# Optimization experiments

Measured on AMD Instinct MI355X. Metric: run time of the kernel, lower is better.

## Reference

```python
import jax, jax.numpy as jnp
import numpy as np

TOL = 5            # proximity_tolerance
DECAY = 0.8        # distance_decay
SWITCH_W = 20.0    # switch_loss_weight


def setup_inputs() -> dict:
    key = jax.random.key(0)
    k1, k2 = jax.random.split(key)
    B, S, C = 512, 8192, 4
    logits = jax.random.normal(k1, (B, S, C), dtype=jnp.float32)
    labels = jax.random.randint(k2, (B, S), 0, 4, dtype=jnp.int32)
    class_weights = jnp.array([1.0, 1.0, SWITCH_W, SWITCH_W], dtype=jnp.float32)
    return {"logits": logits, "labels": labels, "class_weights": class_weights}


def _nearest_dist(mask):
    """Per row: distance from each position to the nearest True in `mask`.
    Returns a large value (> S) where the row has no True. mask: [B, S] bool."""
    B, S = mask.shape
    idx = jnp.arange(S, dtype=jnp.int32)
    big = jnp.int32(4 * S)
    # index of nearest True at-or-before each position (forward cummax)
    prev = jax.lax.cummax(jnp.where(mask, idx, -big), axis=1)
    # index of nearest True at-or-after each position (backward cummin)
    nxt = jnp.flip(jax.lax.cummin(jnp.flip(jnp.where(mask, idx, 3 * big), axis=1), axis=1), axis=1)
    return jnp.minimum(idx - prev, nxt - idx)  # [B, S] int32


def reference(logits, labels, class_weights):
    B, S, C = logits.shape
    safe = jnp.where(labels < 0, 0, labels)  # handle ignore_index=-100
    logp = jax.nn.log_softmax(logits, axis=-1)
    nll = -jnp.take_along_axis(logp, safe[..., None], axis=-1)[..., 0]
    # torch F.cross_entropy(weight=w, reduction='none'): weight[y] * nll, 0 at ignore_index
    ce = jnp.where(labels < 0, 0.0, nll * class_weights[safe])  # [B, S]

    preds = jnp.argmax(logits, axis=-1)

    for c in (2, 3):  # switch-to-auto, switch-to-allo
        tmask = labels == c
        pmask = preds == c
        # predicted switches near (0 < d <= tol) a true switch of same type -> decay
        d_pt = _nearest_dist(tmask)  # dist to nearest true switch (big if none)
        near = (d_pt > 0) & (d_pt <= TOL)
        decay = jnp.where(pmask & near,
                          DECAY ** jnp.minimum(d_pt, TOL).astype(jnp.float32),
                          1.0)
        # true switches: x2 if no predicted switch of this type in the row,
        # x1.5 if nearest predicted switch is farther than tol
        d_tp = _nearest_dist(pmask)  # dist to nearest predicted switch
        any_pred = jnp.any(pmask, axis=1, keepdims=True)
        tfac = jnp.where(tmask,
                         jnp.where(any_pred,
                                   jnp.where(d_tp > TOL, 1.5, 1.0),
                                   2.0),
                         1.0)
        ce = ce * decay * tfac

    valid = (labels >= 0).astype(jnp.float32)
    return (ce * valid).sum() / jnp.maximum(valid.sum(), 1.0)
```

## Files before the change

kernel.cpp:

```cpp
#include <hip/hip_runtime.h>


#define S_LEN 8192
#define NTHREADS 1024
#define NITER (S_LEN / NTHREADS)
#define NWORDS (S_LEN / 32)
#define NWAVES (NTHREADS / 64)

__device__ inline unsigned win11(const unsigned* m, int pos) {
    int bse = pos - 5;
    int j = bse >> 5;
    int off = bse & 31;
    unsigned lo = (j >= 0) ? m[j] : 0u;
    unsigned hi = (j < NWORDS - 1) ? m[j + 1] : 0u;
    unsigned long long c = (unsigned long long)lo | ((unsigned long long)hi << 32);
    return (unsigned)((c >> off) & 0x7FFull);
}

__device__ inline float prox_factor(unsigned tw, unsigned pw, bool anyp) {
    bool tm = (tw >> 5) & 1u;
    bool pm = (pw >> 5) & 1u;
    float f = 1.0f;
    unsigned tn = tw & ~(1u << 5);
    if (pm && !tm && tn) {
        if      (tn & 0x050u) f = 0.8f;
        else if (tn & 0x088u) f = 0.64f;
        else if (tn & 0x104u) f = 0.512f;
        else if (tn & 0x202u) f = 0.4096f;
        else                  f = 0.32768f;
    }
    if (tm) {
        f *= anyp ? (pw ? 1.0f : 1.5f) : 2.0f;
    }
    return f;
}

__global__ __launch_bounds__(NTHREADS)
void prox_loss_main(const float* __restrict__ logits,
                    const int* __restrict__ labels,
                    const float* __restrict__ cw,
                    float* __restrict__ acc) {
    __shared__ float ce_lds[S_LEN];
    __shared__ unsigned t2m[NWORDS], t3m[NWORDS];
    __shared__ unsigned p2m[NWORDS], p3m[NWORDS];
    __shared__ unsigned anyf[2];
    __shared__ float part_s[NWAVES], part_v[NWAVES];

    const int tid = threadIdx.x;
    const int row = blockIdx.x;
    const long base = (long)row * S_LEN;

    if (tid < 2) anyf[tid] = 0u;

    const float w0 = cw[0], w1 = cw[1], w2 = cw[2], w3 = cw[3];

    float local_valid = 0.0f;

    for (int k = 0; k < NITER; ++k) {
        const int pos = k * NTHREADS + tid;
        const long g = base + pos;
        const float4 x = reinterpret_cast<const float4*>(logits)[g];
        const int lab = labels[g];

        int pred = 0; float best = x.x;
        if (x.y > best) { best = x.y; pred = 1; }
        if (x.z > best) { best = x.z; pred = 2; }
        if (x.w > best) { best = x.w; pred = 3; }

        const float m = fmaxf(fmaxf(x.x, x.y), fmaxf(x.z, x.w));
        const float s = expf(x.x - m) + expf(x.y - m) + expf(x.z - m) + expf(x.w - m);
        const float lse = m + logf(s);
        const int safe = (lab < 0) ? 0 : lab;
        const float xl = (safe == 0) ? x.x : (safe == 1) ? x.y : (safe == 2) ? x.z : x.w;
        const float ws = (safe == 0) ? w0  : (safe == 1) ? w1  : (safe == 2) ? w2  : w3;
        const float ce = (lab < 0) ? 0.0f : ws * (lse - xl);
        ce_lds[pos] = ce;
        if (lab >= 0) local_valid += 1.0f;

        const unsigned long long bt2 = __ballot(lab == 2);
        const unsigned long long bt3 = __ballot(lab == 3);
        const unsigned long long bp2 = __ballot(pred == 2);
        const unsigned long long bp3 = __ballot(pred == 3);
        if ((tid & 63) == 0) {
            const int widx = pos >> 5;
            t2m[widx] = (unsigned)bt2; t2m[widx + 1] = (unsigned)(bt2 >> 32);
            t3m[widx] = (unsigned)bt3; t3m[widx + 1] = (unsigned)(bt3 >> 32);
            p2m[widx] = (unsigned)bp2; p2m[widx + 1] = (unsigned)(bp2 >> 32);
            p3m[widx] = (unsigned)bp3; p3m[widx + 1] = (unsigned)(bp3 >> 32);
        }
    }
    __syncthreads();

    if (tid < NWORDS) {
        if (p2m[tid] != 0u) atomicOr(&anyf[0], 1u);
        if (p3m[tid] != 0u) atomicOr(&anyf[1], 1u);
    }
    __syncthreads();
    const bool any2 = anyf[0] != 0u;
    const bool any3 = anyf[1] != 0u;

    float local_sum = 0.0f;
    for (int k = 0; k < NITER; ++k) {
        const int pos = k * NTHREADS + tid;
        float f = ce_lds[pos];
        const unsigned tw2 = win11(t2m, pos), pw2 = win11(p2m, pos);
        const unsigned tw3 = win11(t3m, pos), pw3 = win11(p3m, pos);
        f *= prox_factor(tw2, pw2, any2);
        f *= prox_factor(tw3, pw3, any3);
        local_sum += f;
    }

    for (int o = 32; o > 0; o >>= 1) {
        local_sum   += __shfl_down(local_sum, o);
        local_valid += __shfl_down(local_valid, o);
    }
    const int wv = tid >> 6;
    if ((tid & 63) == 0) { part_s[wv] = local_sum; part_v[wv] = local_valid; }
    __syncthreads();
    if (tid == 0) {
        float ssum = 0.0f, vsum = 0.0f;
        for (int i = 0; i < NWAVES; ++i) { ssum += part_s[i]; vsum += part_v[i]; }
        atomicAdd(&acc[0], ssum);
        atomicAdd(&acc[1], vsum);
    }
}

__global__ void prox_loss_finalize(const float* __restrict__ acc,
                                   float* __restrict__ out) {
    out[0] = acc[0] / fmaxf(acc[1], 1.0f);
}

extern "C" void kernel_launch(void* const* d_in, const int* in_sizes, int n_in,
                              void* d_out, int out_size, void* d_ws, size_t ws_size,
                              hipStream_t stream) {
    const float* logits = (const float*)d_in[0];
    const int*   labels = (const int*)d_in[1];
    const float* cw     = (const float*)d_in[2];
    float* out = (float*)d_out;
    float* acc = (float*)d_ws;

    const int B = in_sizes[1] / S_LEN;

    hipMemsetAsync(acc, 0, 2 * sizeof(float), stream);
    prox_loss_main<<<B, NTHREADS, 0, stream>>>(logits, labels, cw, acc);
    prox_loss_finalize<<<1, 1, 0, stream>>>(acc, out);
}
```

Measured before the change: 116.2 us.

## Keep per-position CE in registers and fuse finalize via last-block atomic

Per-position cross-entropy values are kept in a register array instead of a 32KB shared-memory buffer, reducing LDS use so more blocks can be resident per CU. Softmax uses exp2/log2 with the argmax value as the max. The separate finalize kernel is replaced by a ticket counter where the last block writes the result, removing one launch. This adds register pressure and relies on atomic-read visibility of the accumulators.

```diff
diff --git a/kernel.cpp b/kernel.cpp
--- a/kernel.cpp
+++ b/kernel.cpp
@@ -39,21 +39,24 @@
 void prox_loss_main(const float* __restrict__ logits,
                     const int* __restrict__ labels,
                     const float* __restrict__ cw,
-                    float* __restrict__ acc) {
-    __shared__ float ce_lds[S_LEN];
+                    float* __restrict__ acc,
+                    float* __restrict__ out,
+                    int nblocks) {
     __shared__ unsigned t2m[NWORDS], t3m[NWORDS];
     __shared__ unsigned p2m[NWORDS], p3m[NWORDS];
     __shared__ unsigned anyf[2];
     __shared__ float part_s[NWAVES], part_v[NWAVES];
 
     const int tid = threadIdx.x;
-    const int row = blockIdx.x;
-    const long base = (long)row * S_LEN;
+    const long base = (long)blockIdx.x * S_LEN;
 
     if (tid < 2) anyf[tid] = 0u;
 
     const float w0 = cw[0], w1 = cw[1], w2 = cw[2], w3 = cw[3];
+    const float L2E = 1.4426950408889634f;
+    const float LN2 = 0.6931471805599453f;
 
+    float ce_reg[NITER];
     float local_valid = 0.0f;
 
     for (int k = 0; k < NITER; ++k) {
@@ -67,15 +70,14 @@
         if (x.z > best) { best = x.z; pred = 2; }
         if (x.w > best) { best = x.w; pred = 3; }
 
-        const float m = fmaxf(fmaxf(x.x, x.y), fmaxf(x.z, x.w));
-        const float s = expf(x.x - m) + expf(x.y - m) + expf(x.z - m) + expf(x.w - m);
-        const float lse = m + logf(s);
+        const float s = exp2f((x.x - best) * L2E) + exp2f((x.y - best) * L2E)
+                      + exp2f((x.z - best) * L2E) + exp2f((x.w - best) * L2E);
+        const float lnsum = log2f(s) * LN2;
         const int safe = (lab < 0) ? 0 : lab;
         const float xl = (safe == 0) ? x.x : (safe == 1) ? x.y : (safe == 2) ? x.z : x.w;
         const float ws = (safe == 0) ? w0  : (safe == 1) ? w1  : (safe == 2) ? w2  : w3;
-        const float ce = (lab < 0) ? 0.0f : ws * (lse - xl);
-        ce_lds[pos] = ce;
-        if (lab >= 0) local_valid += 1.0f;
+        ce_reg[k] = (lab < 0) ? 0.0f : ws * (best + lnsum - xl);
+        local_valid += (lab >= 0) ? 1.0f : 0.0f;
 
         const unsigned long long bt2 = __ballot(lab == 2);
         const unsigned long long bt3 = __ballot(lab == 3);
@@ -102,7 +104,7 @@
     float local_sum = 0.0f;
     for (int k = 0; k < NITER; ++k) {
         const int pos = k * NTHREADS + tid;
-        float f = ce_lds[pos];
+        float f = ce_reg[k];
         const unsigned tw2 = win11(t2m, pos), pw2 = win11(p2m, pos);
         const unsigned tw3 = win11(t3m, pos), pw3 = win11(p3m, pos);
         f *= prox_factor(tw2, pw2, any2);
@@ -117,17 +119,20 @@
     const int wv = tid >> 6;
     if ((tid & 63) == 0) { part_s[wv] = local_sum; part_v[wv] = local_valid; }
     __syncthreads();
+
     if (tid == 0) {
         float ssum = 0.0f, vsum = 0.0f;
         for (int i = 0; i < NWAVES; ++i) { ssum += part_s[i]; vsum += part_v[i]; }
         atomicAdd(&acc[0], ssum);
         atomicAdd(&acc[1], vsum);
+        __threadfence();
+        const unsigned t = atomicAdd(reinterpret_cast<unsigned*>(&acc[2]), 1u);
+        if (t == (unsigned)(nblocks - 1)) {
+            const float fs = atomicAdd(&acc[0], 0.0f);
+            const float fv = atomicAdd(&acc[1], 0.0f);
+            out[0] = fs / fmaxf(fv, 1.0f);
+        }
     }
-}
-
-__global__ void prox_loss_finalize(const float* __restrict__ acc,
-                                   float* __restrict__ out) {
-    out[0] = acc[0] / fmaxf(acc[1], 1.0f);
 }
 
 extern "C" void kernel_launch(void* const* d_in, const int* in_sizes, int n_in,
@@ -141,7 +146,6 @@
 
     const int B = in_sizes[1] / S_LEN;
 
-    hipMemsetAsync(acc, 0, 2 * sizeof(float), stream);
-    prox_loss_main<<<B, NTHREADS, 0, stream>>>(logits, labels, cw, acc);
-    prox_loss_finalize<<<1, 1, 0, stream>>>(acc, out);
+    hipMemsetAsync(acc, 0, 3 * sizeof(float), stream);
+    prox_loss_main<<<B, NTHREADS, 0, stream>>>(logits, labels, cw, acc, out, B);
 }
```

Result: slower. 130.9 us (+12.6%).
